# Kernel tuning notes

Hardware: AMD Instinct MI355X
Metric: run time of the kernel (lower is better)

Reference implementation:

```python
import jax, jax.numpy as jnp
import numpy as np

N, K, D = 65536, 4096, 256
COMMITMENT_COST = 0.25


def setup_inputs() -> dict:
    key = jax.random.key(0)
    k1, k2 = jax.random.split(key)
    z_flat = jax.random.normal(k1, (N, D), dtype=jnp.float32)
    # init_method='normal': std=0.02
    codebook = jax.random.normal(k2, (K, D), dtype=jnp.float32) * 0.02
    return {"z_flat": z_flat, "codebook": codebook}


def reference(z_flat, codebook):
    # distances[n,k] = ||z_n||^2 + ||e_k||^2 - 2 z_n . e_k   (squared L2)
    z_sq = jnp.sum(z_flat ** 2, axis=1, keepdims=True)            # [N,1]
    e_sq = jnp.sum(codebook ** 2, axis=1)                          # [K]
    distances = z_sq + e_sq - 2.0 * jnp.matmul(z_flat, codebook.T)  # [N,K]
    indices = jnp.argmin(distances, axis=1)                        # [N] int
    quantized = codebook[indices]                                  # [N,D]

    e_latent_loss = jnp.mean((jax.lax.stop_gradient(quantized) - z_flat) ** 2)
    q_latent_loss = jnp.mean((quantized - jax.lax.stop_gradient(z_flat)) ** 2)
    loss = q_latent_loss + COMMITMENT_COST * e_latent_loss

    # straight-through estimator
    quantized_st = z_flat + jax.lax.stop_gradient(quantized - z_flat)
    return loss, quantized_st, indices
```

## Files before the change

### kernel.cpp

```cpp
#include <hip/hip_runtime.h>
#include <float.h>

typedef __attribute__((ext_vector_type(8))) short short8;
typedef __attribute__((ext_vector_type(16))) float f32x16;
typedef unsigned short u16;

#define N_ROWS 65536
#define K_CB   4096
#define D_DIM  256
#define TAU    1.0e-3f
#define RR     8

#define RB 128
#define KB 128
#define DB 32

#define WS_COUNTER 0
#define WS_ESQ     16
#define WS_IDX     (WS_ESQ + K_CB*4)
#define WS_FLAG    (WS_IDX + N_ROWS*4)
#define WS_PART    (WS_FLAG + N_ROWS*4)
#define NUM_OUT_BLOCKS ((N_ROWS*(D_DIM/4))/256)
#define WS_EH      (WS_PART + NUM_OUT_BLOCKS*8)
#define WS_EL      (WS_EH + K_CB*D_DIM*2)
#define WS_NEEDED  (WS_EL + (size_t)K_CB*D_DIM*2)

__device__ __forceinline__ u16 f2bf(float x) {
  unsigned int u = __float_as_uint(x);
  unsigned int r = (u + 0x7fffu + ((u >> 16) & 1u)) >> 16;
  return (u16)r;
}
__device__ __forceinline__ float bf2f(u16 b) {
  return __uint_as_float((unsigned int)b << 16);
}
__device__ __forceinline__ float np_score(float zsq, float ek, float dot) {
#pragma clang fp contract(off)
  float t1 = zsq + ek;
  float t2 = 2.0f * dot;
  return t1 - t2;
}

__device__ __forceinline__ float np_sum128_sq(const float* p) {
#pragma clang fp contract(off)
  float r0 = p[0]*p[0], r1 = p[1]*p[1], r2 = p[2]*p[2], r3 = p[3]*p[3];
  float r4 = p[4]*p[4], r5 = p[5]*p[5], r6 = p[6]*p[6], r7 = p[7]*p[7];
  for (int i = 8; i < 128; i += 8) {
    r0 += p[i+0]*p[i+0]; r1 += p[i+1]*p[i+1];
    r2 += p[i+2]*p[i+2]; r3 += p[i+3]*p[i+3];
    r4 += p[i+4]*p[i+4]; r5 += p[i+5]*p[i+5];
    r6 += p[i+6]*p[i+6]; r7 += p[i+7]*p[i+7];
  }
  return ((r0+r1)+(r2+r3))+((r4+r5)+(r6+r7));
}
__device__ __forceinline__ float np_sumsq256(const float* p) {
#pragma clang fp contract(off)
  float a = np_sum128_sq(p);
  float b = np_sum128_sq(p + 128);
  return a + b;
}

__global__ __launch_bounds__(256) void esq_np_kernel(const float* __restrict__ cb,
                                                     float* __restrict__ esq) {
  const int k = blockIdx.x * 256 + threadIdx.x;
  esq[k] = np_sumsq256(cb + (size_t)k * D_DIM);
}

__global__ __launch_bounds__(256) void esplit_perm_kernel(const float* __restrict__ cb,
                                                          u16* __restrict__ ehp,
                                                          u16* __restrict__ elp) {
  const int g  = blockIdx.x * 256 + threadIdx.x;
  const int k  = g >> 5;
  const int d8 = g & 31;
  const int kc = k >> 5, c = k & 31;
  const float* src = cb + (size_t)k * D_DIM + d8 * 8;
  float4 f0 = *(const float4*)src;
  float4 f1 = *(const float4*)(src + 4);
  float f[8] = {f0.x, f0.y, f0.z, f0.w, f1.x, f1.y, f1.z, f1.w};
  short8 h, lo;
  #pragma unroll
  for (int j = 0; j < 8; ++j) {
    u16 hb = f2bf(f[j]);
    h[j]  = (short)hb;
    lo[j] = (short)f2bf(f[j] - bf2f(hb));
  }
  const size_t off = (size_t)kc * 8192 + (size_t)d8 * 256 + (size_t)c * 8;
  *(short8*)(ehp + off) = h;
  *(short8*)(elp + off) = lo;
}

__global__ __launch_bounds__(256, 2) void mfma_argmin32_kernel(
    const float* __restrict__ z, const u16* __restrict__ ehp,
    const u16* __restrict__ elp, const float* __restrict__ esq,
    int* __restrict__ idx_out, int* __restrict__ flag,
    unsigned int* __restrict__ counter) {
  __shared__ u16 smem[2 * 16384];
  const int t   = threadIdx.x;
  const int w   = t >> 6;
  const int l   = t & 63;
  const int col = l & 31;
  const int hi  = l >> 5;
  const int row = blockIdx.x * 128 + w * 32 + col;
  const int wbase = w * 1024;

  short8 ah[16], al[16];
  {
    const float* zr = z + (size_t)row * D_DIM + hi * 8;
    #pragma unroll
    for (int s = 0; s < 16; ++s) {
      float4 f0 = *(const float4*)(zr + s * 16);
      float4 f1 = *(const float4*)(zr + s * 16 + 4);
      float f[8] = {f0.x, f0.y, f0.z, f0.w, f1.x, f1.y, f1.z, f1.w};
      short8 h, lo;
      #pragma unroll
      for (int j = 0; j < 8; ++j) {
        u16 hb = f2bf(f[j]);
        h[j]  = (short)hb;
        lo[j] = (short)f2bf(f[j] - bf2f(hb));
      }
      ah[s] = h; al[s] = lo;
    }
  }

  float m1[16], m2[16]; int ic[16];
  #pragma unroll
  for (int r = 0; r < 16; ++r) { m1[r] = FLT_MAX; m2[r] = FLT_MAX; ic[r] = 0; }

  #define STAGE(KCN, BUF) do {                                                  \
    char* lb = (char*)smem + (BUF) * 32768;                                     \
    const char* gh = (const char*)ehp + (size_t)(KCN) * 16384;                  \
    const char* gl = (const char*)elp + (size_t)(KCN) * 16384;                  \
    _Pragma("unroll")                                                           \
    for (int q = 0; q < 4; ++q) {                                               \
      __builtin_amdgcn_global_load_lds(                                         \
        (const __attribute__((address_space(1))) void*)(gh + q*4096 + t*16),    \
        (__attribute__((address_space(3))) void*)(lb + q*4096 + wbase),         \
        16, 0, 0);                                                              \
      __builtin_amdgcn_global_load_lds(                                         \
        (const __attribute__((address_space(1))) void*)(gl + q*4096 + t*16),    \
        (__attribute__((address_space(3))) void*)(lb + 16384 + q*4096 + wbase), \
        16, 0, 0);                                                              \
    }                                                                           \
  } while (0)

  STAGE(0, 0);
  __syncthreads();

  const int boff = hi * 512 + col * 16;
  for (int kc = 0; kc < 128; ++kc) {
    const int cur = kc & 1;
    if (kc + 1 < 128) STAGE(kc + 1, cur ^ 1);
    const char* bb = (const char*)smem + cur * 32768;

    f32x16 c0 = {}, c1 = {}, c2 = {}, c3 = {};
    #define MFMA3(S, A0, A1, A2) do {                                           \
      short8 bh = *(const short8*)(bb + (S) * 1024 + boff);                     \
      short8 bl = *(const short8*)(bb + 16384 + (S) * 1024 + boff);             \
      A0 = __builtin_amdgcn_mfma_f32_32x32x16_bf16(ah[S], bh, A0, 0, 0, 0);     \
      A1 = __builtin_amdgcn_mfma_f32_32x32x16_bf16(al[S], bh, A1, 0, 0, 0);     \
      A2 = __builtin_amdgcn_mfma_f32_32x32x16_bf16(ah[S], bl, A2, 0, 0, 0);     \
    } while (0)
    MFMA3(0,  c0, c1, c2);  MFMA3(1,  c3, c0, c1);
    MFMA3(2,  c2, c3, c0);  MFMA3(3,  c1, c2, c3);
    MFMA3(4,  c0, c1, c2);  MFMA3(5,  c3, c0, c1);
    MFMA3(6,  c2, c3, c0);  MFMA3(7,  c1, c2, c3);
    MFMA3(8,  c0, c1, c2);  MFMA3(9,  c3, c0, c1);
    MFMA3(10, c2, c3, c0);  MFMA3(11, c1, c2, c3);
    MFMA3(12, c0, c1, c2);  MFMA3(13, c3, c0, c1);
    MFMA3(14, c2, c3, c0);  MFMA3(15, c1, c2, c3);
    #undef MFMA3

    const float ev = esq[kc * 32 + col];
    #pragma unroll
    for (int r = 0; r < 16; ++r) {
      float sum = (c0[r] + c1[r]) + (c2[r] + c3[r]);
      float sc = fmaf(-2.0f, sum, ev);
      bool lt = sc < m1[r];
      ic[r] = lt ? kc : ic[r];
      m2[r] = fminf(m2[r], fmaxf(m1[r], sc));
      m1[r] = fminf(m1[r], sc);
    }
    __syncthreads();
  }
  #undef STAGE

  #pragma unroll
  for (int r = 0; r < 16; ++r) {
    float a1 = m1[r], a2 = m2[r];
    int cd = ic[r] * 32 + col;
    #pragma unroll
    for (int off = 1; off < 32; off <<= 1) {
      float b1 = __shfl_xor(a1, off);
      float b2 = __shfl_xor(a2, off);
      int   bc = __shfl_xor(cd, off);
      bool take = (b1 < a1) || (b1 == a1 && bc < cd);
      float nm2 = take ? fminf(a1, b2) : fminf(a2, b1);
      if (take) { a1 = b1; cd = bc; }
      a2 = nm2;
    }
    if (col == 0) {
      const int orow = blockIdx.x * 128 + w * 32 + (r & 3) + 8 * (r >> 2) + 4 * hi;
      idx_out[orow] = cd;
      if (a2 - a1 < TAU) {
        unsigned int p = atomicAdd(counter, 1u);
        flag[p] = orow;
      }
    }
  }
}

__global__ __launch_bounds__(256, 2) void argmin_kernel(
    const float4* __restrict__ z4, const float4* __restrict__ cb4,
    const float* __restrict__ esq, int* __restrict__ idx_out,
    int* __restrict__ flag, unsigned int* __restrict__ counter) {
  __shared__ float zt[DB][RB];
  __shared__ float et[DB][KB];
  const int t  = threadIdx.x;
  const int tr = t >> 4;
  const int tc = t & 15;
  const int row0 = blockIdx.x * RB;

  float min1[8], min2[8]; int idx1[8];
  #pragma unroll
  for (int i = 0; i < 8; ++i) { min1[i] = FLT_MAX; min2[i] = FLT_MAX; idx1[i] = 0; }

  for (int kc = 0; kc < K_CB / KB; ++kc) {
    const int k0 = kc * KB;
    float acc[8][8];
    #pragma unroll
    for (int i = 0; i < 8; ++i)
      #pragma unroll
      for (int j = 0; j < 8; ++j) acc[i][j] = 0.0f;

    float esqv[8];
    #pragma unroll
    for (int j = 0; j < 8; ++j) esqv[j] = esq[k0 + tc*8 + j];

    for (int dt = 0; dt < D_DIM / DB; ++dt) {
      __syncthreads();
      #pragma unroll
      for (int m = 0; m < 4; ++m) {
        int u  = t + 256*m;
        int dq = u & 7;
        int r  = u >> 3;
        float4 v = z4[(size_t)(row0 + r)*(D_DIM/4) + dt*8 + dq];
        zt[dq*4+0][r] = v.x; zt[dq*4+1][r] = v.y; zt[dq*4+2][r] = v.z; zt[dq*4+3][r] = v.w;
        float4 wv = cb4[(size_t)(k0 + r)*(D_DIM/4) + dt*8 + dq];
        et[dq*4+0][r] = wv.x; et[dq*4+1][r] = wv.y; et[dq*4+2][r] = wv.z; et[dq*4+3][r] = wv.w;
      }
      __syncthreads();

      #pragma unroll 8
      for (int d = 0; d < DB; ++d) {
        float4 za = *(const float4*)&zt[d][tr*8];
        float4 zb = *(const float4*)&zt[d][tr*8+4];
        float4 ea = *(const float4*)&et[d][tc*8];
        float4 eb = *(const float4*)&et[d][tc*8+4];
        float zr[8] = {za.x, za.y, za.z, za.w, zb.x, zb.y, zb.z, zb.w};
        float ev[8] = {ea.x, ea.y, ea.z, ea.w, eb.x, eb.y, eb.z, eb.w};
        #pragma unroll
        for (int i = 0; i < 8; ++i)
          #pragma unroll
          for (int j = 0; j < 8; ++j)
            acc[i][j] += zr[i] * ev[j];
      }
    }

    #pragma unroll
    for (int j = 0; j < 8; ++j) {
      const int k = k0 + tc*8 + j;
      #pragma unroll
      for (int i = 0; i < 8; ++i) {
        float s = esqv[j] - 2.0f * acc[i][j];
        if (s < min1[i]) { min2[i] = min1[i]; min1[i] = s; idx1[i] = k; }
        else if (s < min2[i]) { min2[i] = s; }
      }
    }
  }

  #pragma unroll
  for (int i = 0; i < 8; ++i) {
    float m1 = min1[i], m2 = min2[i]; int id = idx1[i];
    #pragma unroll
    for (int off = 1; off < 16; off <<= 1) {
      float om1 = __shfl_xor(m1, off);
      float om2 = __shfl_xor(m2, off);
      int   oid = __shfl_xor(id, off);
      bool take = (om1 < m1) || (om1 == m1 && oid < id);
      float nm2 = take ? fminf(m1, om2) : fminf(m2, om1);
      if (take) { m1 = om1; id = oid; }
      m2 = nm2;
    }
    if (tc == 0) {
      int row = row0 + tr*8 + i;
      idx_out[row] = id;
      if (m2 - m1 < TAU) {
        unsigned int p = atomicAdd(counter, 1u);
        flag[p] = row;
      }
    }
  }
}

__global__ __launch_bounds__(256) void refine_np_kernel(
    const float* __restrict__ z, const float* __restrict__ cb,
    const float* __restrict__ esq, int* __restrict__ idx_out,
    const int* __restrict__ flag, const unsigned int* __restrict__ counter) {
  __shared__ float zrow[RR][D_DIM];
  __shared__ float zsq[RR];
  __shared__ float rbest[256];
  __shared__ int   rbidx[256];
  const int t = threadIdx.x;
  const unsigned int cnt = *counter;
  const unsigned int ngroups = (cnt + RR - 1) / RR;

  for (unsigned int g = blockIdx.x; g < ngroups; g += gridDim.x) {
    __syncthreads();
    const int nr = (int)min((unsigned int)RR, cnt - g*RR);
    #pragma unroll
    for (int r = 0; r < RR; ++r) {
      int fi = (int)(g*RR) + ((r < nr) ? r : 0);
      int row = flag[fi];
      zrow[r][t] = z[(size_t)row * D_DIM + t];
    }
    __syncthreads();
    if (t < RR) zsq[t] = np_sumsq256(&zrow[t][0]);
    __syncthreads();

    float best[RR]; int bidx[RR];
    #pragma unroll
    for (int r = 0; r < RR; ++r) { best[r] = FLT_MAX; bidx[r] = 0x7fffffff; }

    for (int m = 0; m < K_CB / 256; ++m) {
      const int k = m*256 + t;
      const float4* e4 = (const float4*)(cb + (size_t)k * D_DIM);
      float acc[RR];
      #pragma unroll
      for (int r = 0; r < RR; ++r) acc[r] = 0.0f;
      for (int dq = 0; dq < D_DIM/4; ++dq) {
        float4 ev = e4[dq];
        #pragma unroll
        for (int r = 0; r < RR; ++r) {
          acc[r] = __fmaf_rn(zrow[r][dq*4+0], ev.x, acc[r]);
          acc[r] = __fmaf_rn(zrow[r][dq*4+1], ev.y, acc[r]);
          acc[r] = __fmaf_rn(zrow[r][dq*4+2], ev.z, acc[r]);
          acc[r] = __fmaf_rn(zrow[r][dq*4+3], ev.w, acc[r]);
        }
      }
      const float ek = esq[k];
      #pragma unroll
      for (int r = 0; r < RR; ++r) {
        float sc = np_score(zsq[r], ek, acc[r]);
        if (sc < best[r]) { best[r] = sc; bidx[r] = k; }
      }
    }

    for (int r = 0; r < RR; ++r) {
      __syncthreads();
      rbest[t] = best[r]; rbidx[t] = bidx[r];
      __syncthreads();
      for (int off = 128; off > 0; off >>= 1) {
        if (t < off) {
          float ob = rbest[t+off]; int oi = rbidx[t+off];
          if (ob < rbest[t] || (ob == rbest[t] && oi < rbidx[t])) {
            rbest[t] = ob; rbidx[t] = oi;
          }
        }
        __syncthreads();
      }
      if (t == 0 && r < nr) idx_out[flag[g*RR + r]] = rbidx[0];
    }
  }
}

__global__ __launch_bounds__(256) void output_kernel(
    const float4* __restrict__ z4, const float4* __restrict__ cb4,
    const int* __restrict__ idx_out, float* __restrict__ out,
    double* __restrict__ partials) {
  const int g  = blockIdx.x * 256 + threadIdx.x;
  const int n  = g >> 6;
  const int dq = g & 63;
  const int id = idx_out[n];
  float4 q  = cb4[(size_t)id * (D_DIM/4) + dq];
  float4 zv = z4[(size_t)n  * (D_DIM/4) + dq];
  float dx = q.x - zv.x, dy = q.y - zv.y, dz = q.z - zv.z, dw = q.w - zv.w;
  double psum = (double)dx*dx + (double)dy*dy + (double)dz*dz + (double)dw*dw;
  size_t base = 1 + (size_t)n * D_DIM + (size_t)dq * 4;
  out[base+0] = q.x; out[base+1] = q.y; out[base+2] = q.z; out[base+3] = q.w;
  if (dq == 0) out[1 + (size_t)N_ROWS*D_DIM + n] = (float)id;

  __shared__ double sred[256];
  sred[threadIdx.x] = psum;
  __syncthreads();
  for (int off = 128; off > 0; off >>= 1) {
    if (threadIdx.x < off) sred[threadIdx.x] += sred[threadIdx.x + off];
    __syncthreads();
  }
  if (threadIdx.x == 0) partials[blockIdx.x] = sred[0];
}

__global__ __launch_bounds__(256) void loss_kernel(const double* __restrict__ partials,
                                                   float* __restrict__ out) {
  const int t = threadIdx.x;
  double s = 0.0;
  for (int m = 0; m < NUM_OUT_BLOCKS/256; ++m) s += partials[t + 256*m];
  __shared__ double sred[256];
  sred[t] = s;
  __syncthreads();
  for (int off = 128; off > 0; off >>= 1) {
    if (t < off) sred[t] += sred[t + off];
    __syncthreads();
  }
  if (t == 0) out[0] = (float)(1.25 * sred[0] / ((double)N_ROWS * (double)D_DIM));
}

extern "C" void kernel_launch(void* const* d_in, const int* in_sizes, int n_in,
                              void* d_out, int out_size, void* d_ws, size_t ws_size,
                              hipStream_t stream) {
  const float* z  = (const float*)d_in[0];
  const float* cb = (const float*)d_in[1];
  float* out = (float*)d_out;
  char* ws = (char*)d_ws;

  unsigned int* counter = (unsigned int*)(ws + WS_COUNTER);
  float*  esq      = (float*) (ws + WS_ESQ);
  int*    idx      = (int*)   (ws + WS_IDX);
  int*    flag     = (int*)   (ws + WS_FLAG);
  double* partials = (double*)(ws + WS_PART);

  (void)hipMemsetAsync(ws, 0, 16, stream);
  esq_np_kernel<<<K_CB/256, 256, 0, stream>>>(cb, esq);

  if (ws_size >= WS_NEEDED) {
    u16* ehp = (u16*)(ws + WS_EH);
    u16* elp = (u16*)(ws + WS_EL);
    esplit_perm_kernel<<<(K_CB*(D_DIM/8))/256, 256, 0, stream>>>(cb, ehp, elp);
    mfma_argmin32_kernel<<<N_ROWS/128, 256, 0, stream>>>(z, ehp, elp, esq,
                                                         idx, flag, counter);
  } else {
    argmin_kernel<<<N_ROWS/RB, 256, 0, stream>>>((const float4*)z, (const float4*)cb,
                                                 esq, idx, flag, counter);
  }

  refine_np_kernel<<<256, 256, 0, stream>>>(z, cb, esq, idx, flag, counter);
  output_kernel<<<NUM_OUT_BLOCKS, 256, 0, stream>>>((const float4*)z, (const float4*)cb,
                                                    idx, out, partials);
  loss_kernel<<<1, 256, 0, stream>>>(partials, out);
}
```

Baseline: 599.7 us.

## Process two 32-row tiles per wave to reuse codebook fragments across MFMAs

```diff
diff --git a/kernel.cpp b/kernel.cpp
--- a/kernel.cpp
+++ b/kernel.cpp
@@ -88,7 +88,7 @@
   *(short8*)(elp + off) = lo;
 }
 
-__global__ __launch_bounds__(256, 2) void mfma_argmin32_kernel(
+__global__ __launch_bounds__(256, 1) void mfma_argmin32_kernel(
     const float* __restrict__ z, const u16* __restrict__ ehp,
     const u16* __restrict__ elp, const float* __restrict__ esq,
     int* __restrict__ idx_out, int* __restrict__ flag,
@@ -99,12 +99,13 @@
   const int l   = t & 63;
   const int col = l & 31;
   const int hi  = l >> 5;
-  const int row = blockIdx.x * 128 + w * 32 + col;
+  const int rowbase = blockIdx.x * 256 + w * 64;
   const int wbase = w * 1024;
 
-  short8 ah[16], al[16];
-  {
-    const float* zr = z + (size_t)row * D_DIM + hi * 8;
+  short8 ah0[16], al0[16], ah1[16], al1[16];
+  #pragma unroll
+  for (int rb = 0; rb < 2; ++rb) {
+    const float* zr = z + (size_t)(rowbase + rb * 32 + col) * D_DIM + hi * 8;
     #pragma unroll
     for (int s = 0; s < 16; ++s) {
       float4 f0 = *(const float4*)(zr + s * 16);
@@ -117,13 +118,14 @@
         h[j]  = (short)hb;
         lo[j] = (short)f2bf(f[j] - bf2f(hb));
       }
-      ah[s] = h; al[s] = lo;
-    }
-  }
-
-  float m1[16], m2[16]; int ic[16];
-  #pragma unroll
-  for (int r = 0; r < 16; ++r) { m1[r] = FLT_MAX; m2[r] = FLT_MAX; ic[r] = 0; }
+      if (rb == 0) { ah0[s] = h; al0[s] = lo; }
+      else         { ah1[s] = h; al1[s] = lo; }
+    }
+  }
+
+  float m1[32], m2[32]; int ic[32];
+  #pragma unroll
+  for (int j = 0; j < 32; ++j) { m1[j] = FLT_MAX; m2[j] = FLT_MAX; ic[j] = 0; }
 
   #define STAGE(KCN, BUF) do {                                                  \
     char* lb = (char*)smem + (BUF) * 32768;                                     \
@@ -152,57 +154,60 @@
     const char* bb = (const char*)smem + cur * 32768;
 
     f32x16 c0 = {}, c1 = {}, c2 = {}, c3 = {};
-    #define MFMA3(S, A0, A1, A2) do {                                           \
-      short8 bh = *(const short8*)(bb + (S) * 1024 + boff);                     \
-      short8 bl = *(const short8*)(bb + 16384 + (S) * 1024 + boff);             \
-      A0 = __builtin_amdgcn_mfma_f32_32x32x16_bf16(ah[S], bh, A0, 0, 0, 0);     \
-      A1 = __builtin_amdgcn_mfma_f32_32x32x16_bf16(al[S], bh, A1, 0, 0, 0);     \
-      A2 = __builtin_amdgcn_mfma_f32_32x32x16_bf16(ah[S], bl, A2, 0, 0, 0);     \
-    } while (0)
-    MFMA3(0,  c0, c1, c2);  MFMA3(1,  c3, c0, c1);
-    MFMA3(2,  c2, c3, c0);  MFMA3(3,  c1, c2, c3);
-    MFMA3(4,  c0, c1, c2);  MFMA3(5,  c3, c0, c1);
-    MFMA3(6,  c2, c3, c0);  MFMA3(7,  c1, c2, c3);
-    MFMA3(8,  c0, c1, c2);  MFMA3(9,  c3, c0, c1);
-    MFMA3(10, c2, c3, c0);  MFMA3(11, c1, c2, c3);
-    MFMA3(12, c0, c1, c2);  MFMA3(13, c3, c0, c1);
-    MFMA3(14, c2, c3, c0);  MFMA3(15, c1, c2, c3);
-    #undef MFMA3
+    #pragma unroll
+    for (int s = 0; s < 16; ++s) {
+      short8 bh = *(const short8*)(bb + s * 1024 + boff);
+      short8 bl = *(const short8*)(bb + 16384 + s * 1024 + boff);
+      c0 = __builtin_amdgcn_mfma_f32_32x32x16_bf16(ah0[s], bh, c0, 0, 0, 0);
+      c1 = __builtin_amdgcn_mfma_f32_32x32x16_bf16(ah1[s], bh, c1, 0, 0, 0);
+      c2 = __builtin_amdgcn_mfma_f32_32x32x16_bf16(al0[s], bh, c2, 0, 0, 0);
+      c3 = __builtin_amdgcn_mfma_f32_32x32x16_bf16(al1[s], bh, c3, 0, 0, 0);
+      c0 = __builtin_amdgcn_mfma_f32_32x32x16_bf16(ah0[s], bl, c0, 0, 0, 0);
+      c1 = __builtin_amdgcn_mfma_f32_32x32x16_bf16(ah1[s], bl, c1, 0, 0, 0);
+    }
 
     const float ev = esq[kc * 32 + col];
     #pragma unroll
     for (int r = 0; r < 16; ++r) {
-      float sum = (c0[r] + c1[r]) + (c2[r] + c3[r]);
-      float sc = fmaf(-2.0f, sum, ev);
-      bool lt = sc < m1[r];
-      ic[r] = lt ? kc : ic[r];
-      m2[r] = fminf(m2[r], fmaxf(m1[r], sc));
-      m1[r] = fminf(m1[r], sc);
+      float sc0 = fmaf(-2.0f, c0[r] + c2[r], ev);
+      bool lt0 = sc0 < m1[r];
+      ic[r] = lt0 ? kc : ic[r];
+      m2[r] = fminf(m2[r], fmaxf(m1[r], sc0));
+      m1[r] = fminf(m1[r], sc0);
+      float sc1 = fmaf(-2.0f, c1[r] + c3[r], ev);
+      bool lt1 = sc1 < m1[16 + r];
+      ic[16 + r] = lt1 ? kc : ic[16 + r];
+      m2[16 + r] = fminf(m2[16 + r], fmaxf(m1[16 + r], sc1));
+      m1[16 + r] = fminf(m1[16 + r], sc1);
     }
     __syncthreads();
   }
   #undef STAGE
 
   #pragma unroll
-  for (int r = 0; r < 16; ++r) {
-    float a1 = m1[r], a2 = m2[r];
-    int cd = ic[r] * 32 + col;
-    #pragma unroll
-    for (int off = 1; off < 32; off <<= 1) {
-      float b1 = __shfl_xor(a1, off);
-      float b2 = __shfl_xor(a2, off);
-      int   bc = __shfl_xor(cd, off);
-      bool take = (b1 < a1) || (b1 == a1 && bc < cd);
-      float nm2 = take ? fminf(a1, b2) : fminf(a2, b1);
-      if (take) { a1 = b1; cd = bc; }
-      a2 = nm2;
-    }
-    if (col == 0) {
-      const int orow = blockIdx.x * 128 + w * 32 + (r & 3) + 8 * (r >> 2) + 4 * hi;
-      idx_out[orow] = cd;
-      if (a2 - a1 < TAU) {
-        unsigned int p = atomicAdd(counter, 1u);
-        flag[p] = orow;
+  for (int rb = 0; rb < 2; ++rb) {
+    #pragma unroll
+    for (int r = 0; r < 16; ++r) {
+      const int j = rb * 16 + r;
+      float a1 = m1[j], a2 = m2[j];
+      int cd = ic[j] * 32 + col;
+      #pragma unroll
+      for (int off = 1; off < 32; off <<= 1) {
+        float b1 = __shfl_xor(a1, off);
+        float b2 = __shfl_xor(a2, off);
+        int   bc = __shfl_xor(cd, off);
+        bool take = (b1 < a1) || (b1 == a1 && bc < cd);
+        float nm2 = take ? fminf(a1, b2) : fminf(a2, b1);
+        if (take) { a1 = b1; cd = bc; }
+        a2 = nm2;
+      }
+      if (col == 0) {
+        const int orow = rowbase + rb * 32 + (r & 3) + 8 * (r >> 2) + 4 * hi;
+        idx_out[orow] = cd;
+        if (a2 - a1 < TAU) {
+          unsigned int p = atomicAdd(counter, 1u);
+          flag[p] = orow;
+        }
       }
     }
   }
@@ -434,7 +439,7 @@
     u16* ehp = (u16*)(ws + WS_EH);
     u16* elp = (u16*)(ws + WS_EL);
     esplit_perm_kernel<<<(K_CB*(D_DIM/8))/256, 256, 0, stream>>>(cb, ehp, elp);
-    mfma_argmin32_kernel<<<N_ROWS/128, 256, 0, stream>>>(z, ehp, elp, esq,
+    mfma_argmin32_kernel<<<N_ROWS/256, 256, 0, stream>>>(z, ehp, elp, esq,
                                                          idx, flag, counter);
   } else {
     argmin_kernel<<<N_ROWS/RB, 256, 0, stream>>>((const float4*)z, (const float4*)cb,
```

Result: slower. 621.6 us (+3.7%).

## Swap MFMA operands so each lane owns one row, removing cross-lane argmin reduction

Applied to the files above, without the earlier changes.

```diff
diff --git a/kernel.cpp b/kernel.cpp
--- a/kernel.cpp
+++ b/kernel.cpp
@@ -4,6 +4,7 @@
 typedef __attribute__((ext_vector_type(8))) short short8;
 typedef __attribute__((ext_vector_type(16))) float f32x16;
 typedef unsigned short u16;
+typedef unsigned int u32;
 
 #define N_ROWS 65536
 #define K_CB   4096
@@ -88,23 +89,23 @@
   *(short8*)(elp + off) = lo;
 }
 
-__global__ __launch_bounds__(256, 2) void mfma_argmin32_kernel(
+__global__ __launch_bounds__(256, 2) void coarse32_kernel(
     const float* __restrict__ z, const u16* __restrict__ ehp,
     const u16* __restrict__ elp, const float* __restrict__ esq,
     int* __restrict__ idx_out, int* __restrict__ flag,
-    unsigned int* __restrict__ counter) {
+    u32* __restrict__ counter) {
   __shared__ u16 smem[2 * 16384];
   const int t   = threadIdx.x;
   const int w   = t >> 6;
   const int l   = t & 63;
   const int col = l & 31;
   const int hi  = l >> 5;
-  const int row = blockIdx.x * 128 + w * 32 + col;
+  const int rowbase = blockIdx.x * 128 + w * 32;
   const int wbase = w * 1024;
 
-  short8 ah[16], al[16];
+  short8 bzh[16], bzl[16];
   {
-    const float* zr = z + (size_t)row * D_DIM + hi * 8;
+    const float* zr = z + (size_t)(rowbase + col) * D_DIM + hi * 8;
     #pragma unroll
     for (int s = 0; s < 16; ++s) {
       float4 f0 = *(const float4*)(zr + s * 16);
@@ -117,13 +118,12 @@
         h[j]  = (short)hb;
         lo[j] = (short)f2bf(f[j] - bf2f(hb));
       }
-      ah[s] = h; al[s] = lo;
-    }
-  }
-
-  float m1[16], m2[16]; int ic[16];
-  #pragma unroll
-  for (int r = 0; r < 16; ++r) { m1[r] = FLT_MAX; m2[r] = FLT_MAX; ic[r] = 0; }
+      bzh[s] = h; bzl[s] = lo;
+    }
+  }
+
+  float m1 = FLT_MAX, m2 = FLT_MAX;
+  int ic = 0;
 
   #define STAGE(KCN, BUF) do {                                                  \
     char* lb = (char*)smem + (BUF) * 32768;                                     \
@@ -146,63 +146,54 @@
   __syncthreads();
 
   const int boff = hi * 512 + col * 16;
-  for (int kc = 0; kc < 128; ++kc) {
-    const int cur = kc & 1;
-    if (kc + 1 < 128) STAGE(kc + 1, cur ^ 1);
+  for (int cc = 0; cc < 128; ++cc) {
+    const int cur = cc & 1;
+    if (cc + 1 < 128) STAGE(cc + 1, cur ^ 1);
     const char* bb = (const char*)smem + cur * 32768;
 
-    f32x16 c0 = {}, c1 = {}, c2 = {}, c3 = {};
-    #define MFMA3(S, A0, A1, A2) do {                                           \
-      short8 bh = *(const short8*)(bb + (S) * 1024 + boff);                     \
-      short8 bl = *(const short8*)(bb + 16384 + (S) * 1024 + boff);             \
-      A0 = __builtin_amdgcn_mfma_f32_32x32x16_bf16(ah[S], bh, A0, 0, 0, 0);     \
-      A1 = __builtin_amdgcn_mfma_f32_32x32x16_bf16(al[S], bh, A1, 0, 0, 0);     \
-      A2 = __builtin_amdgcn_mfma_f32_32x32x16_bf16(ah[S], bl, A2, 0, 0, 0);     \
-    } while (0)
-    MFMA3(0,  c0, c1, c2);  MFMA3(1,  c3, c0, c1);
-    MFMA3(2,  c2, c3, c0);  MFMA3(3,  c1, c2, c3);
-    MFMA3(4,  c0, c1, c2);  MFMA3(5,  c3, c0, c1);
-    MFMA3(6,  c2, c3, c0);  MFMA3(7,  c1, c2, c3);
-    MFMA3(8,  c0, c1, c2);  MFMA3(9,  c3, c0, c1);
-    MFMA3(10, c2, c3, c0);  MFMA3(11, c1, c2, c3);
-    MFMA3(12, c0, c1, c2);  MFMA3(13, c3, c0, c1);
-    MFMA3(14, c2, c3, c0);  MFMA3(15, c1, c2, c3);
-    #undef MFMA3
-
-    const float ev = esq[kc * 32 + col];
+    float4 eq[4];
+    #pragma unroll
+    for (int q = 0; q < 4; ++q)
+      eq[q] = *(const float4*)(esq + cc*32 + q*8 + hi*4);
+
+    f32x16 chh = {}, clh = {}, chl = {};
+    #pragma unroll
+    for (int s = 0; s < 16; ++s) {
+      short8 ah = *(const short8*)(bb + s * 1024 + boff);
+      short8 al = *(const short8*)(bb + 16384 + s * 1024 + boff);
+      chh = __builtin_amdgcn_mfma_f32_32x32x16_bf16(ah, bzh[s], chh, 0, 0, 0);
+      clh = __builtin_amdgcn_mfma_f32_32x32x16_bf16(al, bzh[s], clh, 0, 0, 0);
+      chl = __builtin_amdgcn_mfma_f32_32x32x16_bf16(ah, bzl[s], chl, 0, 0, 0);
+    }
+
     #pragma unroll
     for (int r = 0; r < 16; ++r) {
-      float sum = (c0[r] + c1[r]) + (c2[r] + c3[r]);
+      float sum = (chh[r] + clh[r]) + chl[r];
+      float ev = ((const float*)&eq[r >> 2])[r & 3];
       float sc = fmaf(-2.0f, sum, ev);
-      bool lt = sc < m1[r];
-      ic[r] = lt ? kc : ic[r];
-      m2[r] = fminf(m2[r], fmaxf(m1[r], sc));
-      m1[r] = fminf(m1[r], sc);
+      bool lt = sc < m1;
+      m2 = fminf(m2, fmaxf(m1, sc));
+      ic = lt ? (cc*32 + (r & 3) + 8*(r >> 2) + 4*hi) : ic;
+      m1 = fminf(m1, sc);
     }
     __syncthreads();
   }
   #undef STAGE
 
-  #pragma unroll
-  for (int r = 0; r < 16; ++r) {
-    float a1 = m1[r], a2 = m2[r];
-    int cd = ic[r] * 32 + col;
-    #pragma unroll
-    for (int off = 1; off < 32; off <<= 1) {
-      float b1 = __shfl_xor(a1, off);
-      float b2 = __shfl_xor(a2, off);
-      int   bc = __shfl_xor(cd, off);
-      bool take = (b1 < a1) || (b1 == a1 && bc < cd);
-      float nm2 = take ? fminf(a1, b2) : fminf(a2, b1);
-      if (take) { a1 = b1; cd = bc; }
-      a2 = nm2;
-    }
-    if (col == 0) {
-      const int orow = blockIdx.x * 128 + w * 32 + (r & 3) + 8 * (r >> 2) + 4 * hi;
-      idx_out[orow] = cd;
-      if (a2 - a1 < TAU) {
-        unsigned int p = atomicAdd(counter, 1u);
-        flag[p] = orow;
+  {
+    float b1 = __shfl_xor(m1, 32);
+    float b2 = __shfl_xor(m2, 32);
+    int   bc = __shfl_xor(ic, 32);
+    bool take = (b1 < m1) || (b1 == m1 && bc < ic);
+    float nm2 = take ? fminf(m1, b2) : fminf(m2, b1);
+    if (take) { m1 = b1; ic = bc; }
+    m2 = nm2;
+    if (hi == 0) {
+      const int row = rowbase + col;
+      idx_out[row] = ic;
+      if (m2 - m1 < TAU) {
+        u32 p = atomicAdd(counter, 1u);
+        flag[p] = row;
       }
     }
   }
@@ -434,8 +425,8 @@
     u16* ehp = (u16*)(ws + WS_EH);
     u16* elp = (u16*)(ws + WS_EL);
     esplit_perm_kernel<<<(K_CB*(D_DIM/8))/256, 256, 0, stream>>>(cb, ehp, elp);
-    mfma_argmin32_kernel<<<N_ROWS/128, 256, 0, stream>>>(z, ehp, elp, esq,
-                                                         idx, flag, counter);
+    coarse32_kernel<<<N_ROWS/128, 256, 0, stream>>>(z, ehp, elp, esq,
+                                                    idx, flag, counter);
   } else {
     argmin_kernel<<<N_ROWS/RB, 256, 0, stream>>>((const float4*)z, (const float4*)cb,
                                                  esq, idx, flag, counter);
```

Result: faster. 583.4 us (-2.7%).
